# Optimization experiments

Hardware: AMD Instinct MI355X
Metric: run time of the kernel (lower is better)

## Reference

```python
import jax, jax.numpy as jnp
import numpy as np

KAPPA = 1.0
SIGMA = 0.3
EPS = 1e-5  # torch BatchNorm1d default eps


def _bn(y, g, b):
    # training-mode batch norm: biased batch statistics over the batch axis
    mu = jnp.mean(y, axis=0)
    var = jnp.mean((y - mu) ** 2, axis=0)
    return g * (y - mu) * jax.lax.rsqrt(var + EPS) + b


def _hid(x, W, b, g, be):
    # Linear -> BatchNorm1d -> ReLU
    return jax.nn.relu(_bn(x @ W + b, g, be))


def setup_inputs() -> dict:
    key = jax.random.key(0)
    ks = jax.random.split(key, 12)
    B, D, H, T = 2048, 256, 266, 51  # H = dim + 10
    S = T - 1
    sc = jnp.float32(0.1)
    f32 = jnp.float32
    inp = {}
    inp["x"] = jax.random.normal(ks[0], (B, D), f32)
    inp["dW"] = jax.random.normal(ks[1], (S, B, D), f32)   # hoisted per-step noise xi
    inp["law"] = jax.random.normal(ks[2], (S, D), f32)
    inp["timegrid"] = jnp.linspace(0.0, 1.0, T).astype(f32)
    # per-timestep MLP stacks (i_h1 / h1_h2 / h2_o)
    inp["W1"] = sc * jax.random.normal(ks[3], (S, D, H), f32)
    inp["b1"] = jnp.zeros((S, H), f32)
    inp["g1"] = jnp.ones((S, H), f32)
    inp["be1"] = jnp.zeros((S, H), f32)
    inp["W2"] = sc * jax.random.normal(ks[4], (S, H, H), f32)
    inp["b2"] = jnp.zeros((S, H), f32)
    inp["g2"] = jnp.ones((S, H), f32)
    inp["be2"] = jnp.zeros((S, H), f32)
    inp["W3"] = sc * jax.random.normal(ks[5], (S, H, D), f32)
    inp["b3"] = jnp.zeros((S, D), f32)
    # v0 network (v0_i_h1 / v0_h1_h2 / v0_h2_o, all Linear+BN+ReLU)
    inp["Wv1"] = sc * jax.random.normal(ks[6], (D, H), f32)
    inp["bv1"] = jnp.zeros((H,), f32)
    inp["gv1"] = jnp.ones((H,), f32)
    inp["bev1"] = jnp.zeros((H,), f32)
    inp["Wv2"] = sc * jax.random.normal(ks[7], (H, H), f32)
    inp["bv2"] = jnp.zeros((H,), f32)
    inp["gv2"] = jnp.ones((H,), f32)
    inp["bev2"] = jnp.zeros((H,), f32)
    inp["Wv3"] = sc * jax.random.normal(ks[8], (H, 1), f32)
    inp["bv3"] = jnp.zeros((1,), f32)
    inp["gv3"] = jnp.ones((1,), f32)
    inp["bev3"] = jnp.zeros((1,), f32)
    return inp


def reference(x, dW, law, timegrid,
              W1, b1, g1, be1, W2, b2, g2, be2, W3, b3,
              Wv1, bv1, gv1, bev1, Wv2, bv2, gv2, bev2, Wv3, bv3, gv3, bev3):
    hgrid = jnp.diff(timegrid)  # [S]
    # v0 network evaluated on the initial state (note: last stage is also Linear+BN+ReLU)
    v0 = _hid(_hid(_hid(x, Wv1, bv1, gv1, bev1), Wv2, bv2, gv2, bev2), Wv3, bv3, gv3, bev3)  # [B,1]

    def step(carry, xs):
        xc, v = carry
        w1, bb1, gg1, bbe1, w2, bb2, gg2, bbe2, w3, bb3, li, dw, h = xs
        h1 = _hid(xc, w1, bb1, gg1, bbe1)
        h2 = _hid(h1, w2, bb2, gg2, bbe2)
        grad = h2 @ w3 + bb3                                   # [B,D]
        # f = kappa^2/2 * ||x - law_i||^2 + 1/2 * ||alpha||^2,  alpha = -grad
        f = 0.5 * KAPPA ** 2 * jnp.sum((xc - li) ** 2, axis=1) + 0.5 * jnp.sum(grad ** 2, axis=1)
        noise = SIGMA * jnp.sqrt(h) * dw                       # [B,D]
        # diag(grad @ noise^T) == rowwise dot product: O(B*D) instead of O(B^2*D)
        v = v - (f * h)[:, None] + jnp.sum(grad * noise, axis=1, keepdims=True)
        xc = xc - grad * h + noise
        return (xc, v), None

    (x_final, v), _ = jax.lax.scan(
        step, (x, v0),
        (W1, b1, g1, be1, W2, b2, g2, be2, W3, b3, law, dW, hgrid))
    return v  # [B,1]; (x_final and the path are byproducts of the same scan)
```

## Files before the change

kernel.cpp:

```cpp
#include <hip/hip_runtime.h>
#include <hip/hip_bf16.h>


#define BATCH 2048
#define DD    256
#define HH    266
#define HP    272
#define SS    50
#define BN_EPS 1e-5f
#define SIG   0.3f
#define AS_STRIDE 296

#define XC_OFF 0
#define Y1_OFF 524288
#define Y2_OFF 1081344
#define V_OFF  1638400
#define S1_OFF 1640448
#define S2_OFF 1649152
#define S1V_OFF 1657856
#define S2V_OFF 1662208
#define SV_OFF  1666560
#define WQ_OFF  1666576

#define W1S 69632
#define W2S 78336
#define W3S 73728
#define W1Q_OFF 0
#define W2Q_OFF 3481600
#define W3Q_OFF 7398400
#define WV1Q_OFF 11084800
#define WV2Q_OFF 11154432

#define BAR_OFF 7283200

typedef unsigned short ushort_t;
using short8 = __attribute__((ext_vector_type(8))) short;
using f32x4  = __attribute__((ext_vector_type(4))) float;

__device__ __forceinline__ ushort_t f2b(float f) {
    unsigned u = __float_as_uint(f);
    unsigned r = u + 0x7FFF + ((u >> 16) & 1);
    return (ushort_t)(r >> 16);
}

__device__ __forceinline__ float ld_coh(const float* p) {
    return __hip_atomic_load((const float*)p, __ATOMIC_RELAXED, __HIP_MEMORY_SCOPE_AGENT);
}

__device__ __forceinline__ void prefetch16(const void* p, int n16, int tid) {
    const f32x4* q = (const f32x4*)p;
    for (int i = tid; i < n16; i += 512) {
        f32x4 t = q[i];
        asm volatile("" :: "v"(t));
    }
}

__global__ __launch_bounds__(256) void k_conv(const float* __restrict__ src,
                                              ushort_t* __restrict__ dst,
                                              int K, int N, int KT, int NT,
                                              long total) {
    long t = (long)blockIdx.x * 256 + threadIdx.x;
    if (t >= total) return;
    int per = KT * NT * 512;
    int step = (int)(t / per);
    int e = (int)(t - (long)step * per);
    int kt = e / (NT * 512);
    int r = e - kt * NT * 512;
    int nt = r / 512;
    int r2 = r & 511;
    int lane = r2 >> 3;
    int j = r2 & 7;
    int k = kt * 32 + (lane >> 4) * 8 + j;
    int n = nt * 16 + (lane & 15);
    float v = (k < K && n < N) ? src[(size_t)step * K * N + (size_t)k * N + n] : 0.f;
    dst[t] = f2b(v);
}

__global__ __launch_bounds__(256) void k_pre(float* __restrict__ ws) {
    unsigned* bar = (unsigned*)(ws + BAR_OFF);
    for (int i = threadIdx.x; i < 512; i += 256) atomicExch(bar + i, 0u);
}

__device__ __forceinline__ void grid_bar(unsigned* bar, unsigned gen, int bid) {
    __syncthreads();
    if (threadIdx.x == 0) {
        unsigned* leaf = bar + (bid & 7) * 32;
        unsigned* root = bar + 256;
        unsigned* rel  = bar + 288;
        bool done = false;
        unsigned a = __hip_atomic_fetch_add(leaf, 1u, __ATOMIC_RELAXED, __HIP_MEMORY_SCOPE_AGENT);
        if (a == gen * 32u + 31u) {
            unsigned r = __hip_atomic_fetch_add(root, 1u, __ATOMIC_RELAXED, __HIP_MEMORY_SCOPE_AGENT);
            if (r == gen * 8u + 7u) {
                __hip_atomic_store(rel, gen + 1u, __ATOMIC_RELAXED, __HIP_MEMORY_SCOPE_AGENT);
                done = true;
            }
        }
        if (!done) {
            while (__hip_atomic_load(rel, __ATOMIC_RELAXED, __HIP_MEMORY_SCOPE_AGENT) < gen + 1u)
                __builtin_amdgcn_s_sleep(1);
        }
        asm volatile("" ::: "memory");
    }
    __syncthreads();
}

__device__ __forceinline__ void compute_ac_coh(const float* __restrict__ si,
                                               const float* __restrict__ g,
                                               const float* __restrict__ be,
                                               float (*AC)[HP]) {
    int t = threadIdx.x;
    if (t < HP) {
        float a = 0.f, c = 0.f;
        if (t < HH) {
            float s = 0.f, q = 0.f;
            #pragma unroll
            for (int r = 0; r < 8; ++r) {
                s += ld_coh(si + r * 544 + t);
                q += ld_coh(si + r * 544 + 272 + t);
            }
            float mu  = s * (1.0f / 2048.0f);
            float var = q * (1.0f / 2048.0f) - mu * mu;
            float rs  = rsqrtf(fmaxf(var, 0.0f) + BN_EPS);
            a = g[t] * rs;
            c = be[t] - mu * a;
        }
        AC[0][t] = a;
        AC[1][t] = c;
    }
}

__device__ __forceinline__ void dev_lin8(
    int bid, int mode, int KT, const float* __restrict__ xsrc, int xld,
    const float* __restrict__ stats_in, const float* __restrict__ g,
    const float* __restrict__ be,
    const ushort_t* __restrict__ Wq, const float* __restrict__ bias,
    float* __restrict__ yout, float* __restrict__ stats_out,
    float* __restrict__ zero_ptr,
    ushort_t* __restrict__ As, float (*AC)[HP])
{
    const int tid  = threadIdx.x;
    const int lane = tid & 63;
    const int wv   = tid >> 6;
    const int quad = lane >> 4;
    const int l15  = lane & 15;
    const int row0 = bid * 8;

    if (zero_ptr != nullptr) {
        int z = bid * 512 + tid;
        if (z < 4352) atomicExch(zero_ptr + z, 0.0f);
    }

    if (mode == 2) { compute_ac_coh(stats_in, g, be, AC); __syncthreads(); }

    const int PAIRS = KT * 16;
    for (int idx = tid; idx < 8 * PAIRS; idx += 512) {
        int m  = idx / PAIRS;
        int kk = (idx - m * PAIRS) * 2;
        float v0, v1;
        if (mode == 2) {
            v0 = (kk < HH)   ? fmaxf(fmaf(AC[0][kk],   xsrc[(size_t)(row0+m)*xld + kk],   AC[1][kk]),   0.f) : 0.f;
            v1 = (kk+1 < HH) ? fmaxf(fmaf(AC[0][kk+1], xsrc[(size_t)(row0+m)*xld + kk+1], AC[1][kk+1]), 0.f) : 0.f;
        } else {
            v0 = xsrc[(size_t)(row0+m)*xld + kk];
            v1 = xsrc[(size_t)(row0+m)*xld + kk + 1];
        }
        ((unsigned int*)As)[m * (AS_STRIDE/2) + (kk >> 1)] =
            (unsigned int)f2b(v0) | ((unsigned int)f2b(v1) << 16);
    }
    __syncthreads();

    f32x4 acc[3];
    #pragma unroll
    for (int i = 0; i < 3; ++i) acc[i] = (f32x4){0.f, 0.f, 0.f, 0.f};

    for (int kt = 0; kt < KT; ++kt) {
        short8 af = *(const short8*)(&As[l15 * AS_STRIDE + kt * 32 + quad * 8]);
        const ushort_t* wp = Wq + ((size_t)(kt * 17 + wv)) * 512 + lane * 8;
        #pragma unroll
        for (int i = 0; i < 3; ++i) {
            if (i < 2 || wv == 0) {
                short8 bf = *(const short8*)(wp + (size_t)i * 8 * 512);
                acc[i] = __builtin_amdgcn_mfma_f32_16x16x32_bf16(af, bf, acc[i], 0, 0, 0);
            }
        }
    }

    #pragma unroll
    for (int i = 0; i < 3; ++i) {
        if (i == 2 && wv != 0) continue;
        int t = wv + 8 * i;
        int col = t * 16 + l15;
        float bj = (col < HH) ? bias[col] : 0.f;
        float y0 = acc[i][0] + bj, y1 = acc[i][1] + bj;
        float y2 = acc[i][2] + bj, y3 = acc[i][3] + bj;
        if (quad < 2) {
            yout[(size_t)(row0 + quad*4 + 0) * HP + col] = y0;
            yout[(size_t)(row0 + quad*4 + 1) * HP + col] = y1;
            yout[(size_t)(row0 + quad*4 + 2) * HP + col] = y2;
            yout[(size_t)(row0 + quad*4 + 3) * HP + col] = y3;
        }
        float sp = (quad < 2) ? (y0 + y1 + y2 + y3) : 0.f;
        float sq = (quad < 2) ? (y0*y0 + y1*y1 + y2*y2 + y3*y3) : 0.f;
        sp += __shfl_xor(sp, 16); sp += __shfl_xor(sp, 32);
        sq += __shfl_xor(sq, 16); sq += __shfl_xor(sq, 32);
        if (quad == 0 && col < HH) {
            float* spp = stats_out + (bid & 7) * 544;
            atomicAdd(spp + col, sp);
            atomicAdd(spp + 272 + col, sq);
        }
    }
}

__device__ __forceinline__ void dev_fused8(
    int bid,
    const float* __restrict__ y2g, const float* __restrict__ stats_in,
    const float* __restrict__ g2, const float* __restrict__ be2,
    const ushort_t* __restrict__ W3q, const float* __restrict__ b3,
    const float* __restrict__ law, const float* __restrict__ dWs,
    const float* __restrict__ tg, int s, int doP1,
    float* __restrict__ xc, float* __restrict__ vv, float* __restrict__ outv,
    const ushort_t* __restrict__ W1q, const float* __restrict__ b1n,
    float* __restrict__ Y1, float* __restrict__ stats_out,
    float* __restrict__ zero_ptr,
    ushort_t* __restrict__ As, float (*AC)[HP], float* __restrict__ red)
{
    const int tid  = threadIdx.x;
    const int lane = tid & 63;
    const int wv   = tid >> 6;
    const int quad = lane >> 4;
    const int l15  = lane & 15;
    const int row0 = bid * 8;

    if (zero_ptr != nullptr) {
        int z = bid * 512 + tid;
        if (z < 4352) atomicExch(zero_ptr + z, 0.0f);
    }

    compute_ac_coh(stats_in, g2, be2, AC);
    __syncthreads();

    for (int idx = tid; idx < 8 * 144; idx += 512) {
        int m  = idx / 144;
        int kk = (idx - m * 144) * 2;
        float v0 = (kk < HH)   ? fmaxf(fmaf(AC[0][kk],   y2g[(size_t)(row0+m)*HP + kk],   AC[1][kk]),   0.f) : 0.f;
        float v1 = (kk+1 < HH) ? fmaxf(fmaf(AC[0][kk+1], y2g[(size_t)(row0+m)*HP + kk+1], AC[1][kk+1]), 0.f) : 0.f;
        ((unsigned int*)As)[m * (AS_STRIDE/2) + (kk >> 1)] =
            (unsigned int)f2b(v0) | ((unsigned int)f2b(v1) << 16);
    }
    __syncthreads();

    f32x4 acc[2];
    acc[0] = (f32x4){0.f,0.f,0.f,0.f};
    acc[1] = (f32x4){0.f,0.f,0.f,0.f};
    for (int kt = 0; kt < 9; ++kt) {
        short8 af = *(const short8*)(&As[l15 * AS_STRIDE + kt * 32 + quad * 8]);
        const ushort_t* wp = W3q + ((size_t)(kt * 16 + wv)) * 512 + lane * 8;
        acc[0] = __builtin_amdgcn_mfma_f32_16x16x32_bf16(af, *(const short8*)(wp),           acc[0], 0, 0, 0);
        acc[1] = __builtin_amdgcn_mfma_f32_16x16x32_bf16(af, *(const short8*)(wp + 8 * 512), acc[1], 0, 0, 0);
    }

    const float h   = tg[s + 1] - tg[s];
    const float srt = SIG * sqrtf(h);
    float grad[2][4], xcv[2][4], dwv[2][4];
    float sxr[4] = {0,0,0,0}, sgr[4] = {0,0,0,0}, sgnr[4] = {0,0,0,0};
    #pragma unroll
    for (int i = 0; i < 2; ++i) {
        int col = (wv + 8*i) * 16 + l15;
        #pragma unroll
        for (int r = 0; r < 4; ++r) {
            float gd = acc[i][r] + b3[col];
            grad[i][r] = gd;
            xcv[i][r] = 0.f; dwv[i][r] = 0.f;
            if (quad < 2) {
                int row = row0 + quad * 4 + r;
                float xv = xc[(size_t)row * DD + col];
                float dw = dWs[(size_t)row * DD + col];
                float d  = xv - law[col];
                xcv[i][r] = xv; dwv[i][r] = dw;
                sxr[r]  = fmaf(d, d, sxr[r]);
                sgr[r]  = fmaf(gd, gd, sgr[r]);
                sgnr[r] = fmaf(gd, dw, sgnr[r]);
            }
        }
    }
    #pragma unroll
    for (int off = 1; off < 16; off <<= 1) {
        #pragma unroll
        for (int r = 0; r < 4; ++r) {
            sxr[r]  += __shfl_xor(sxr[r],  off);
            sgr[r]  += __shfl_xor(sgr[r],  off);
            sgnr[r] += __shfl_xor(sgnr[r], off);
        }
    }
    if (l15 == 0 && quad < 2) {
        #pragma unroll
        for (int r = 0; r < 4; ++r) {
            int rr = quad * 4 + r;
            red[(wv * 8 + rr) * 3 + 0] = sxr[r];
            red[(wv * 8 + rr) * 3 + 1] = sgr[r];
            red[(wv * 8 + rr) * 3 + 2] = sgnr[r];
        }
    }
    __syncthreads();

    if (tid < 8) {
        float sx = 0.f, sg = 0.f, sgn = 0.f;
        #pragma unroll
        for (int w = 0; w < 8; ++w) {
            sx  += red[(w * 8 + tid) * 3 + 0];
            sg  += red[(w * 8 + tid) * 3 + 1];
            sgn += red[(w * 8 + tid) * 3 + 2];
        }
        int row = row0 + tid;
        float f  = 0.5f * (sx + sg);
        float vn = vv[row] - f * h + srt * sgn;
        vv[row] = vn;
        if (s == SS - 1) outv[row] = vn;
    }

    #pragma unroll
    for (int i = 0; i < 2; ++i) {
        int col = (wv + 8*i) * 16 + l15;
        if (quad < 2) {
            #pragma unroll
            for (int r = 0; r < 4; ++r) {
                int row = row0 + quad * 4 + r;
                float xn = xcv[i][r] - grad[i][r] * h + srt * dwv[i][r];
                xc[(size_t)row * DD + col] = xn;
                if (doP1) As[(quad * 4 + r) * AS_STRIDE + col] = f2b(xn);
            }
        }
    }
    if (!doP1) return;
    __syncthreads();

    f32x4 acc2[3];
    #pragma unroll
    for (int i = 0; i < 3; ++i) acc2[i] = (f32x4){0.f, 0.f, 0.f, 0.f};
    for (int kt = 0; kt < 8; ++kt) {
        short8 af = *(const short8*)(&As[l15 * AS_STRIDE + kt * 32 + quad * 8]);
        const ushort_t* wp = W1q + ((size_t)(kt * 17 + wv)) * 512 + lane * 8;
        #pragma unroll
        for (int i = 0; i < 3; ++i) {
            if (i < 2 || wv == 0) {
                short8 bf = *(const short8*)(wp + (size_t)i * 8 * 512);
                acc2[i] = __builtin_amdgcn_mfma_f32_16x16x32_bf16(af, bf, acc2[i], 0, 0, 0);
            }
        }
    }
    #pragma unroll
    for (int i = 0; i < 3; ++i) {
        if (i == 2 && wv != 0) continue;
        int t = wv + 8 * i;
        int col = t * 16 + l15;
        float bj = (col < HH) ? b1n[col] : 0.f;
        float y0 = acc2[i][0] + bj, y1 = acc2[i][1] + bj;
        float y2 = acc2[i][2] + bj, y3 = acc2[i][3] + bj;
        if (quad < 2) {
            Y1[(size_t)(row0 + quad*4 + 0) * HP + col] = y0;
            Y1[(size_t)(row0 + quad*4 + 1) * HP + col] = y1;
            Y1[(size_t)(row0 + quad*4 + 2) * HP + col] = y2;
            Y1[(size_t)(row0 + quad*4 + 3) * HP + col] = y3;
        }
        float sp = (quad < 2) ? (y0 + y1 + y2 + y3) : 0.f;
        float sq = (quad < 2) ? (y0*y0 + y1*y1 + y2*y2 + y3*y3) : 0.f;
        sp += __shfl_xor(sp, 16); sp += __shfl_xor(sp, 32);
        sq += __shfl_xor(sq, 16); sq += __shfl_xor(sq, 32);
        if (quad == 0 && col < HH) {
            float* spp = stats_out + (bid & 7) * 544;
            atomicAdd(spp + col, sp);
            atomicAdd(spp + 272 + col, sq);
        }
    }
}

__device__ __forceinline__ void dev_v0l3_8(
    int bid, const float* __restrict__ y2, const float* __restrict__ stats_in,
    const float* __restrict__ gv, const float* __restrict__ bev,
    const float* __restrict__ wv3, const float* __restrict__ bv3,
    float* __restrict__ vout, float* __restrict__ sv,
    float (*AC)[HP], float* __restrict__ xtra)
{
    const int tid = threadIdx.x;
    compute_ac_coh(stats_in, gv, bev, AC);
    __syncthreads();

    const int r   = tid >> 6;
    const int ln  = tid & 63;
    const int row = bid * 8 + r;
    int k0 = ln * 5, k1 = k0 + 5;
    if (k1 > HH) k1 = HH;
    float acc = 0.0f;
    for (int k = k0; k < k1; ++k) {
        float y  = y2[(size_t)row * HP + k];
        float a2 = fmaxf(fmaf(AC[0][k], y, AC[1][k]), 0.0f);
        acc = fmaf(a2, wv3[k], acc);
    }
    #pragma unroll
    for (int off = 1; off < 64; off <<= 1) acc += __shfl_xor(acc, off);
    if (ln == 0) {
        float y = acc + bv3[0];
        vout[row] = y;
        xtra[r] = y;
        xtra[8 + r] = y * y;
    }
    __syncthreads();
    if (tid == 0) {
        float s = 0.f, q = 0.f;
        #pragma unroll
        for (int i = 0; i < 8; ++i) { s += xtra[i]; q += xtra[8 + i]; }
        atomicAdd(sv, s);
        atomicAdd(sv + 1, q);
    }
}

__device__ __forceinline__ void dev_v0fin8(int bid, float* __restrict__ v,
                                           const float* __restrict__ sv,
                                           const float* __restrict__ gv3,
                                           const float* __restrict__ bev3) {
    if (threadIdx.x < 8) {
        float s0 = ld_coh(sv);
        float s1 = ld_coh(sv + 1);
        float mu  = s0 * (1.0f / 2048.0f);
        float var = s1 * (1.0f / 2048.0f) - mu * mu;
        float rs  = rsqrtf(fmaxf(var, 0.0f) + BN_EPS);
        int row = bid * 8 + threadIdx.x;
        float y = v[row];
        v[row] = fmaxf(gv3[0] * (y - mu) * rs + bev3[0], 0.0f);
    }
}

__global__ __launch_bounds__(512) void k_persist(
    const float* __restrict__ x, const float* __restrict__ dW,
    const float* __restrict__ law, const float* __restrict__ tg,
    const float* __restrict__ b1, const float* __restrict__ g1, const float* __restrict__ be1,
    const float* __restrict__ b2, const float* __restrict__ g2, const float* __restrict__ be2,
    const float* __restrict__ b3,
    const float* __restrict__ bv1, const float* __restrict__ gv1, const float* __restrict__ bev1,
    const float* __restrict__ bv2, const float* __restrict__ gv2, const float* __restrict__ bev2,
    const float* __restrict__ Wv3, const float* __restrict__ bv3,
    const float* __restrict__ gv3, const float* __restrict__ bev3,
    float* __restrict__ ws, float* __restrict__ out)
{
    __shared__ ushort_t As[16 * AS_STRIDE];
    __shared__ float AC[2][HP];
    __shared__ float XTRA[256];

    const int bid = blockIdx.x;
    const int tid = threadIdx.x;

    float* xc  = ws + XC_OFF;
    float* Y1  = ws + Y1_OFF;
    float* Y2  = ws + Y2_OFF;
    float* V   = ws + V_OFF;
    float* S1  = ws + S1_OFF;
    float* S2  = ws + S2_OFF;
    float* S1v = ws + S1V_OFF;
    float* S2v = ws + S2V_OFF;
    float* SV  = ws + SV_OFF;
    ushort_t* WQ = (ushort_t*)(ws + WQ_OFF);
    ushort_t* W1q  = WQ + W1Q_OFF;
    ushort_t* W2q  = WQ + W2Q_OFF;
    ushort_t* W3q  = WQ + W3Q_OFF;
    ushort_t* Wv1q = WQ + WV1Q_OFF;
    ushort_t* Wv2q = WQ + WV2Q_OFF;
    unsigned* bar  = (unsigned*)(ws + BAR_OFF);

    unsigned gen = 0;
    const int sl = (bid >> 3) & 31;

    for (int i = tid; i < 2048; i += 512)
        xc[bid * 2048 + i] = x[bid * 2048 + i];
    {
        int z = bid * 512 + tid;
        if (z < 26128) atomicExch(S1 + z, 0.0f);
    }
    for (int i = tid; i < 8 * AS_STRIDE; i += 512)
        As[8 * AS_STRIDE + i] = 0;
    grid_bar(bar, gen, bid); gen++;

    dev_lin8(bid, 0, 8, x, DD, nullptr, nullptr, nullptr,
             Wv1q, bv1, Y1, S1v, nullptr, As, AC);
    grid_bar(bar, gen, bid); gen++;

    dev_lin8(bid, 2, 9, Y1, HP, S1v, gv1, bev1,
             Wv2q, bv2, Y2, S2v, nullptr, As, AC);
    grid_bar(bar, gen, bid); gen++;

    dev_v0l3_8(bid, Y2, S2v, gv2, bev2, Wv3, bv3, V, SV, AC, XTRA);
    grid_bar(bar, gen, bid); gen++;

    dev_v0fin8(bid, V, SV, gv3, bev3);
    dev_lin8(bid, 0, 8, x, DD, nullptr, nullptr, nullptr,
             W1q, b1, Y1, S1, nullptr, As, AC);
    prefetch16((const char*)W2q + sl * 4896, 306, tid);
    grid_bar(bar, gen, bid); gen++;

    for (int s = 0; s < SS; ++s) {
        int p = s & 1;
        dev_lin8(bid, 2, 9, Y1, HP, S1 + p * 4352,
                 g1 + s * HH, be1 + s * HH,
                 W2q + (size_t)s * W2S, b2 + s * HH,
                 Y2, S2 + p * 4352, S1 + (1 - p) * 4352, As, AC);
        prefetch16(dW + (size_t)s * BATCH * DD + (size_t)bid * 2048, 512, tid);
        prefetch16((const char*)(W3q + (size_t)s * W3S) + sl * 4608, 288, tid);
        if (s + 1 < SS)
            prefetch16((const char*)(W1q + (size_t)(s + 1) * W1S) + sl * 4352, 272, tid);
        grid_bar(bar, gen, bid); gen++;

        int sn = (s + 1 < SS) ? s + 1 : 0;
        dev_fused8(bid, Y2, S2 + p * 4352,
                   g2 + s * HH, be2 + s * HH,
                   W3q + (size_t)s * W3S, b3 + s * DD,
                   law + s * DD, dW + (size_t)s * BATCH * DD,
                   tg, s, (s < SS - 1) ? 1 : 0,
                   xc, V, out,
                   W1q + (size_t)sn * W1S, b1 + sn * HH,
                   Y1, S1 + ((s + 1) & 1) * 4352,
                   S2 + (1 - p) * 4352, As, AC, XTRA);
        if (s + 1 < SS)
            prefetch16((const char*)(W2q + (size_t)(s + 1) * W2S) + sl * 4896, 306, tid);
        grid_bar(bar, gen, bid); gen++;
    }
}

extern "C" void kernel_launch(void* const* d_in, const int* in_sizes, int n_in,
                              void* d_out, int out_size, void* d_ws, size_t ws_size,
                              hipStream_t stream)
{
    (void)in_sizes; (void)n_in; (void)out_size; (void)ws_size;
    const float* x    = (const float*)d_in[0];
    const float* dW   = (const float*)d_in[1];
    const float* law  = (const float*)d_in[2];
    const float* tg   = (const float*)d_in[3];
    const float* W1   = (const float*)d_in[4];
    const float* b1   = (const float*)d_in[5];
    const float* g1   = (const float*)d_in[6];
    const float* be1  = (const float*)d_in[7];
    const float* W2   = (const float*)d_in[8];
    const float* b2   = (const float*)d_in[9];
    const float* g2   = (const float*)d_in[10];
    const float* be2  = (const float*)d_in[11];
    const float* W3   = (const float*)d_in[12];
    const float* b3   = (const float*)d_in[13];
    const float* Wv1  = (const float*)d_in[14];
    const float* bv1  = (const float*)d_in[15];
    const float* gv1  = (const float*)d_in[16];
    const float* bev1 = (const float*)d_in[17];
    const float* Wv2  = (const float*)d_in[18];
    const float* bv2  = (const float*)d_in[19];
    const float* gv2  = (const float*)d_in[20];
    const float* bev2 = (const float*)d_in[21];
    const float* Wv3  = (const float*)d_in[22];
    const float* bv3  = (const float*)d_in[23];
    const float* gv3  = (const float*)d_in[24];
    const float* bev3 = (const float*)d_in[25];

    float* ws = (float*)d_ws;
    ushort_t* WQ = (ushort_t*)(ws + WQ_OFF);
    ushort_t* W1q  = WQ + W1Q_OFF;
    ushort_t* W2q  = WQ + W2Q_OFF;
    ushort_t* W3q  = WQ + W3Q_OFF;
    ushort_t* Wv1q = WQ + WV1Q_OFF;
    ushort_t* Wv2q = WQ + WV2Q_OFF;
    float* out = (float*)d_out;

    k_pre<<<1, 256, 0, stream>>>(ws);
    k_conv<<<13600, 256, 0, stream>>>(W1,  W1q,  DD, HH, 8, 17, (long)SS * W1S);
    k_conv<<<15300, 256, 0, stream>>>(W2,  W2q,  HH, HH, 9, 17, (long)SS * W2S);
    k_conv<<<14400, 256, 0, stream>>>(W3,  W3q,  HH, DD, 9, 16, (long)SS * W3S);
    k_conv<<<272,   256, 0, stream>>>(Wv1, Wv1q, DD, HH, 8, 17, (long)W1S);
    k_conv<<<306,   256, 0, stream>>>(Wv2, Wv2q, HH, HH, 9, 17, (long)W2S);

    k_persist<<<256, 512, 0, stream>>>(
        x, dW, law, tg,
        b1, g1, be1, b2, g2, be2, b3,
        bv1, gv1, bev1, bv2, gv2, bev2,
        Wv3, bv3, gv3, bev3,
        ws, out);
}
```

Measured before the change: 1.394 ms.

## Use 16-row tiles on 128 blocks and keep activations and state in LDS

Halves the persistent grid from 256 to 128 blocks, so each block now owns 16 batch rows and fills the full 16-row MFMA tile instead of wasting half of it. The per-block activations Y1/Y2 and the state xc now stay in shared memory instead of going through global workspace round trips between stages. The grid barrier leaf count changes to match 16 blocks per leaf. In exchange, LDS use per block grows, each block carries twice the row work, and only half as many CUs take part, so the per-stage latency between barriers may rise.

```diff
diff --git a/kernel.cpp b/kernel.cpp
--- a/kernel.cpp
+++ b/kernel.cpp
@@ -89,7 +89,7 @@
         unsigned* rel  = bar + 288;
         bool done = false;
         unsigned a = __hip_atomic_fetch_add(leaf, 1u, __ATOMIC_RELAXED, __HIP_MEMORY_SCOPE_AGENT);
-        if (a == gen * 32u + 31u) {
+        if (a == gen * 16u + 15u) {
             unsigned r = __hip_atomic_fetch_add(root, 1u, __ATOMIC_RELAXED, __HIP_MEMORY_SCOPE_AGENT);
             if (r == gen * 8u + 7u) {
                 __hip_atomic_store(rel, gen + 1u, __ATOMIC_RELAXED, __HIP_MEMORY_SCOPE_AGENT);
@@ -130,12 +130,15 @@
     }
 }
 
-__device__ __forceinline__ void dev_lin8(
-    int bid, int mode, int KT, const float* __restrict__ xsrc, int xld,
+__device__ __forceinline__ void dev_lin16(
+    int bid, int mode, int KT,
+    const float* __restrict__ gsrc,
+    const float* __restrict__ lsrc,
     const float* __restrict__ stats_in, const float* __restrict__ g,
     const float* __restrict__ be,
     const ushort_t* __restrict__ Wq, const float* __restrict__ bias,
-    float* __restrict__ yout, float* __restrict__ stats_out,
+    float* __restrict__ ylds,
+    float* __restrict__ stats_out,
     float* __restrict__ zero_ptr,
     ushort_t* __restrict__ As, float (*AC)[HP])
 {
@@ -144,7 +147,7 @@
     const int wv   = tid >> 6;
     const int quad = lane >> 4;
     const int l15  = lane & 15;
-    const int row0 = bid * 8;
+    const int row0 = bid * 16;
 
     if (zero_ptr != nullptr) {
         int z = bid * 512 + tid;
@@ -154,16 +157,16 @@
     if (mode == 2) { compute_ac_coh(stats_in, g, be, AC); __syncthreads(); }
 
     const int PAIRS = KT * 16;
-    for (int idx = tid; idx < 8 * PAIRS; idx += 512) {
+    for (int idx = tid; idx < 16 * PAIRS; idx += 512) {
         int m  = idx / PAIRS;
         int kk = (idx - m * PAIRS) * 2;
         float v0, v1;
         if (mode == 2) {
-            v0 = (kk < HH)   ? fmaxf(fmaf(AC[0][kk],   xsrc[(size_t)(row0+m)*xld + kk],   AC[1][kk]),   0.f) : 0.f;
-            v1 = (kk+1 < HH) ? fmaxf(fmaf(AC[0][kk+1], xsrc[(size_t)(row0+m)*xld + kk+1], AC[1][kk+1]), 0.f) : 0.f;
+            v0 = (kk < HH)   ? fmaxf(fmaf(AC[0][kk],   lsrc[m * HP + kk],   AC[1][kk]),   0.f) : 0.f;
+            v1 = (kk+1 < HH) ? fmaxf(fmaf(AC[0][kk+1], lsrc[m * HP + kk+1], AC[1][kk+1]), 0.f) : 0.f;
         } else {
-            v0 = xsrc[(size_t)(row0+m)*xld + kk];
-            v1 = xsrc[(size_t)(row0+m)*xld + kk + 1];
+            v0 = gsrc[(size_t)(row0 + m) * DD + kk];
+            v1 = gsrc[(size_t)(row0 + m) * DD + kk + 1];
         }
         ((unsigned int*)As)[m * (AS_STRIDE/2) + (kk >> 1)] =
             (unsigned int)f2b(v0) | ((unsigned int)f2b(v1) << 16);
@@ -194,14 +197,12 @@
         float bj = (col < HH) ? bias[col] : 0.f;
         float y0 = acc[i][0] + bj, y1 = acc[i][1] + bj;
         float y2 = acc[i][2] + bj, y3 = acc[i][3] + bj;
-        if (quad < 2) {
-            yout[(size_t)(row0 + quad*4 + 0) * HP + col] = y0;
-            yout[(size_t)(row0 + quad*4 + 1) * HP + col] = y1;
-            yout[(size_t)(row0 + quad*4 + 2) * HP + col] = y2;
-            yout[(size_t)(row0 + quad*4 + 3) * HP + col] = y3;
-        }
-        float sp = (quad < 2) ? (y0 + y1 + y2 + y3) : 0.f;
-        float sq = (quad < 2) ? (y0*y0 + y1*y1 + y2*y2 + y3*y3) : 0.f;
+        ylds[(quad*4 + 0) * HP + col] = y0;
+        ylds[(quad*4 + 1) * HP + col] = y1;
+        ylds[(quad*4 + 2) * HP + col] = y2;
+        ylds[(quad*4 + 3) * HP + col] = y3;
+        float sp = y0 + y1 + y2 + y3;
+        float sq = y0*y0 + y1*y1 + y2*y2 + y3*y3;
         sp += __shfl_xor(sp, 16); sp += __shfl_xor(sp, 32);
         sq += __shfl_xor(sq, 16); sq += __shfl_xor(sq, 32);
         if (quad == 0 && col < HH) {
@@ -212,16 +213,19 @@
     }
 }
 
-__device__ __forceinline__ void dev_fused8(
+__device__ __forceinline__ void dev_fused16(
     int bid,
-    const float* __restrict__ y2g, const float* __restrict__ stats_in,
+    const float* __restrict__ y2l,
+    const float* __restrict__ stats_in,
     const float* __restrict__ g2, const float* __restrict__ be2,
     const ushort_t* __restrict__ W3q, const float* __restrict__ b3,
     const float* __restrict__ law, const float* __restrict__ dWs,
     const float* __restrict__ tg, int s, int doP1,
-    float* __restrict__ xc, float* __restrict__ vv, float* __restrict__ outv,
+    float* __restrict__ xcl,
+    float* __restrict__ vv, float* __restrict__ outv,
     const ushort_t* __restrict__ W1q, const float* __restrict__ b1n,
-    float* __restrict__ Y1, float* __restrict__ stats_out,
+    float* __restrict__ y1l,
+    float* __restrict__ stats_out,
     float* __restrict__ zero_ptr,
     ushort_t* __restrict__ As, float (*AC)[HP], float* __restrict__ red)
 {
@@ -230,7 +234,7 @@
     const int wv   = tid >> 6;
     const int quad = lane >> 4;
     const int l15  = lane & 15;
-    const int row0 = bid * 8;
+    const int row0 = bid * 16;
 
     if (zero_ptr != nullptr) {
         int z = bid * 512 + tid;
@@ -240,11 +244,11 @@
     compute_ac_coh(stats_in, g2, be2, AC);
     __syncthreads();
 
-    for (int idx = tid; idx < 8 * 144; idx += 512) {
+    for (int idx = tid; idx < 16 * 144; idx += 512) {
         int m  = idx / 144;
         int kk = (idx - m * 144) * 2;
-        float v0 = (kk < HH)   ? fmaxf(fmaf(AC[0][kk],   y2g[(size_t)(row0+m)*HP + kk],   AC[1][kk]),   0.f) : 0.f;
-        float v1 = (kk+1 < HH) ? fmaxf(fmaf(AC[0][kk+1], y2g[(size_t)(row0+m)*HP + kk+1], AC[1][kk+1]), 0.f) : 0.f;
+        float v0 = (kk < HH)   ? fmaxf(fmaf(AC[0][kk],   y2l[m * HP + kk],   AC[1][kk]),   0.f) : 0.f;
+        float v1 = (kk+1 < HH) ? fmaxf(fmaf(AC[0][kk+1], y2l[m * HP + kk+1], AC[1][kk+1]), 0.f) : 0.f;
         ((unsigned int*)As)[m * (AS_STRIDE/2) + (kk >> 1)] =
             (unsigned int)f2b(v0) | ((unsigned int)f2b(v1) << 16);
     }
@@ -269,19 +273,15 @@
         int col = (wv + 8*i) * 16 + l15;
         #pragma unroll
         for (int r = 0; r < 4; ++r) {
+            int rl = quad * 4 + r;
             float gd = acc[i][r] + b3[col];
-            grad[i][r] = gd;
-            xcv[i][r] = 0.f; dwv[i][r] = 0.f;
-            if (quad < 2) {
-                int row = row0 + quad * 4 + r;
-                float xv = xc[(size_t)row * DD + col];
-                float dw = dWs[(size_t)row * DD + col];
-                float d  = xv - law[col];
-                xcv[i][r] = xv; dwv[i][r] = dw;
-                sxr[r]  = fmaf(d, d, sxr[r]);
-                sgr[r]  = fmaf(gd, gd, sgr[r]);
-                sgnr[r] = fmaf(gd, dw, sgnr[r]);
-            }
+            float xv = xcl[rl * DD + col];
+            float dw = dWs[(size_t)(row0 + rl) * DD + col];
+            float d  = xv - law[col];
+            grad[i][r] = gd; xcv[i][r] = xv; dwv[i][r] = dw;
+            sxr[r]  = fmaf(d, d, sxr[r]);
+            sgr[r]  = fmaf(gd, gd, sgr[r]);
+            sgnr[r] = fmaf(gd, dw, sgnr[r]);
         }
     }
     #pragma unroll
@@ -293,24 +293,24 @@
             sgnr[r] += __shfl_xor(sgnr[r], off);
         }
     }
-    if (l15 == 0 && quad < 2) {
+    if (l15 == 0) {
         #pragma unroll
         for (int r = 0; r < 4; ++r) {
             int rr = quad * 4 + r;
-            red[(wv * 8 + rr) * 3 + 0] = sxr[r];
-            red[(wv * 8 + rr) * 3 + 1] = sgr[r];
-            red[(wv * 8 + rr) * 3 + 2] = sgnr[r];
-        }
-    }
-    __syncthreads();
-
-    if (tid < 8) {
+            red[(wv * 16 + rr) * 3 + 0] = sxr[r];
+            red[(wv * 16 + rr) * 3 + 1] = sgr[r];
+            red[(wv * 16 + rr) * 3 + 2] = sgnr[r];
+        }
+    }
+    __syncthreads();
+
+    if (tid < 16) {
         float sx = 0.f, sg = 0.f, sgn = 0.f;
         #pragma unroll
         for (int w = 0; w < 8; ++w) {
-            sx  += red[(w * 8 + tid) * 3 + 0];
-            sg  += red[(w * 8 + tid) * 3 + 1];
-            sgn += red[(w * 8 + tid) * 3 + 2];
+            sx  += red[(w * 16 + tid) * 3 + 0];
+            sg  += red[(w * 16 + tid) * 3 + 1];
+            sgn += red[(w * 16 + tid) * 3 + 2];
         }
         int row = row0 + tid;
         float f  = 0.5f * (sx + sg);
@@ -322,14 +322,12 @@
     #pragma unroll
     for (int i = 0; i < 2; ++i) {
         int col = (wv + 8*i) * 16 + l15;
-        if (quad < 2) {
-            #pragma unroll
-            for (int r = 0; r < 4; ++r) {
-                int row = row0 + quad * 4 + r;
-                float xn = xcv[i][r] - grad[i][r] * h + srt * dwv[i][r];
-                xc[(size_t)row * DD + col] = xn;
-                if (doP1) As[(quad * 4 + r) * AS_STRIDE + col] = f2b(xn);
-            }
+        #pragma unroll
+        for (int r = 0; r < 4; ++r) {
+            int rl = quad * 4 + r;
+            float xn = xcv[i][r] - grad[i][r] * h + srt * dwv[i][r];
+            xcl[rl * DD + col] = xn;
+            if (doP1) As[rl * AS_STRIDE + col] = f2b(xn);
         }
     }
     if (!doP1) return;
@@ -357,14 +355,12 @@
         float bj = (col < HH) ? b1n[col] : 0.f;
         float y0 = acc2[i][0] + bj, y1 = acc2[i][1] + bj;
         float y2 = acc2[i][2] + bj, y3 = acc2[i][3] + bj;
-        if (quad < 2) {
-            Y1[(size_t)(row0 + quad*4 + 0) * HP + col] = y0;
-            Y1[(size_t)(row0 + quad*4 + 1) * HP + col] = y1;
-            Y1[(size_t)(row0 + quad*4 + 2) * HP + col] = y2;
-            Y1[(size_t)(row0 + quad*4 + 3) * HP + col] = y3;
-        }
-        float sp = (quad < 2) ? (y0 + y1 + y2 + y3) : 0.f;
-        float sq = (quad < 2) ? (y0*y0 + y1*y1 + y2*y2 + y3*y3) : 0.f;
+        y1l[(quad*4 + 0) * HP + col] = y0;
+        y1l[(quad*4 + 1) * HP + col] = y1;
+        y1l[(quad*4 + 2) * HP + col] = y2;
+        y1l[(quad*4 + 3) * HP + col] = y3;
+        float sp = y0 + y1 + y2 + y3;
+        float sq = y0*y0 + y1*y1 + y2*y2 + y3*y3;
         sp += __shfl_xor(sp, 16); sp += __shfl_xor(sp, 32);
         sq += __shfl_xor(sq, 16); sq += __shfl_xor(sq, 32);
         if (quad == 0 && col < HH) {
@@ -375,8 +371,8 @@
     }
 }
 
-__device__ __forceinline__ void dev_v0l3_8(
-    int bid, const float* __restrict__ y2, const float* __restrict__ stats_in,
+__device__ __forceinline__ void dev_v0l3_16(
+    int bid, const float* __restrict__ y2l, const float* __restrict__ stats_in,
     const float* __restrict__ gv, const float* __restrict__ bev,
     const float* __restrict__ wv3, const float* __restrict__ bv3,
     float* __restrict__ vout, float* __restrict__ sv,
@@ -386,46 +382,45 @@
     compute_ac_coh(stats_in, gv, bev, AC);
     __syncthreads();
 
-    const int r   = tid >> 6;
-    const int ln  = tid & 63;
-    const int row = bid * 8 + r;
-    int k0 = ln * 5, k1 = k0 + 5;
+    const int r   = tid >> 5;
+    const int ks  = tid & 31;
+    int k0 = ks * 9, k1 = k0 + 9;
     if (k1 > HH) k1 = HH;
     float acc = 0.0f;
     for (int k = k0; k < k1; ++k) {
-        float y  = y2[(size_t)row * HP + k];
+        float y  = y2l[r * HP + k];
         float a2 = fmaxf(fmaf(AC[0][k], y, AC[1][k]), 0.0f);
         acc = fmaf(a2, wv3[k], acc);
     }
     #pragma unroll
-    for (int off = 1; off < 64; off <<= 1) acc += __shfl_xor(acc, off);
-    if (ln == 0) {
+    for (int off = 1; off < 32; off <<= 1) acc += __shfl_xor(acc, off);
+    if (ks == 0) {
         float y = acc + bv3[0];
-        vout[row] = y;
+        vout[bid * 16 + r] = y;
         xtra[r] = y;
-        xtra[8 + r] = y * y;
+        xtra[16 + r] = y * y;
     }
     __syncthreads();
     if (tid == 0) {
         float s = 0.f, q = 0.f;
         #pragma unroll
-        for (int i = 0; i < 8; ++i) { s += xtra[i]; q += xtra[8 + i]; }
+        for (int i = 0; i < 16; ++i) { s += xtra[i]; q += xtra[16 + i]; }
         atomicAdd(sv, s);
         atomicAdd(sv + 1, q);
     }
 }
 
-__device__ __forceinline__ void dev_v0fin8(int bid, float* __restrict__ v,
-                                           const float* __restrict__ sv,
-                                           const float* __restrict__ gv3,
-                                           const float* __restrict__ bev3) {
-    if (threadIdx.x < 8) {
+__device__ __forceinline__ void dev_v0fin16(int bid, float* __restrict__ v,
+                                            const float* __restrict__ sv,
+                                            const float* __restrict__ gv3,
+                                            const float* __restrict__ bev3) {
+    if (threadIdx.x < 16) {
         float s0 = ld_coh(sv);
         float s1 = ld_coh(sv + 1);
         float mu  = s0 * (1.0f / 2048.0f);
         float var = s1 * (1.0f / 2048.0f) - mu * mu;
         float rs  = rsqrtf(fmaxf(var, 0.0f) + BN_EPS);
-        int row = bid * 8 + threadIdx.x;
+        int row = bid * 16 + threadIdx.x;
         float y = v[row];
         v[row] = fmaxf(gv3[0] * (y - mu) * rs + bev3[0], 0.0f);
     }
@@ -445,14 +440,14 @@
 {
     __shared__ ushort_t As[16 * AS_STRIDE];
     __shared__ float AC[2][HP];
-    __shared__ float XTRA[256];
+    __shared__ float Y1s[16 * HP];
+    __shared__ float Y2s[16 * HP];
+    __shared__ float XCs[16 * DD];
+    __shared__ float XTRA[384];
 
     const int bid = blockIdx.x;
     const int tid = threadIdx.x;
 
-    float* xc  = ws + XC_OFF;
-    float* Y1  = ws + Y1_OFF;
-    float* Y2  = ws + Y2_OFF;
     float* V   = ws + V_OFF;
     float* S1  = ws + S1_OFF;
     float* S2  = ws + S2_OFF;
@@ -468,59 +463,57 @@
     unsigned* bar  = (unsigned*)(ws + BAR_OFF);
 
     unsigned gen = 0;
-    const int sl = (bid >> 3) & 31;
-
-    for (int i = tid; i < 2048; i += 512)
-        xc[bid * 2048 + i] = x[bid * 2048 + i];
+    const int sl = (bid >> 3) & 15;
+
+    for (int i = tid; i < 16 * DD; i += 512)
+        XCs[i] = x[(size_t)bid * 16 * DD + i];
     {
         int z = bid * 512 + tid;
         if (z < 26128) atomicExch(S1 + z, 0.0f);
     }
-    for (int i = tid; i < 8 * AS_STRIDE; i += 512)
-        As[8 * AS_STRIDE + i] = 0;
     grid_bar(bar, gen, bid); gen++;
 
-    dev_lin8(bid, 0, 8, x, DD, nullptr, nullptr, nullptr,
-             Wv1q, bv1, Y1, S1v, nullptr, As, AC);
+    dev_lin16(bid, 0, 8, x, nullptr, nullptr, nullptr, nullptr,
+              Wv1q, bv1, Y1s, S1v, nullptr, As, AC);
     grid_bar(bar, gen, bid); gen++;
 
-    dev_lin8(bid, 2, 9, Y1, HP, S1v, gv1, bev1,
-             Wv2q, bv2, Y2, S2v, nullptr, As, AC);
+    dev_lin16(bid, 2, 9, nullptr, Y1s, S1v, gv1, bev1,
+              Wv2q, bv2, Y2s, S2v, nullptr, As, AC);
     grid_bar(bar, gen, bid); gen++;
 
-    dev_v0l3_8(bid, Y2, S2v, gv2, bev2, Wv3, bv3, V, SV, AC, XTRA);
+    dev_v0l3_16(bid, Y2s, S2v, gv2, bev2, Wv3, bv3, V, SV, AC, XTRA);
     grid_bar(bar, gen, bid); gen++;
 
-    dev_v0fin8(bid, V, SV, gv3, bev3);
-    dev_lin8(bid, 0, 8, x, DD, nullptr, nullptr, nullptr,
-             W1q, b1, Y1, S1, nullptr, As, AC);
-    prefetch16((const char*)W2q + sl * 4896, 306, tid);
+    dev_v0fin16(bid, V, SV, gv3, bev3);
+    dev_lin16(bid, 0, 8, x, nullptr, nullptr, nullptr, nullptr,
+              W1q, b1, Y1s, S1, nullptr, As, AC);
+    prefetch16((const char*)W2q + sl * 9792, 612, tid);
     grid_bar(bar, gen, bid); gen++;
 
     for (int s = 0; s < SS; ++s) {
         int p = s & 1;
-        dev_lin8(bid, 2, 9, Y1, HP, S1 + p * 4352,
-                 g1 + s * HH, be1 + s * HH,
-                 W2q + (size_t)s * W2S, b2 + s * HH,
-                 Y2, S2 + p * 4352, S1 + (1 - p) * 4352, As, AC);
-        prefetch16(dW + (size_t)s * BATCH * DD + (size_t)bid * 2048, 512, tid);
-        prefetch16((const char*)(W3q + (size_t)s * W3S) + sl * 4608, 288, tid);
+        dev_lin16(bid, 2, 9, nullptr, Y1s, S1 + p * 4352,
+                  g1 + s * HH, be1 + s * HH,
+                  W2q + (size_t)s * W2S, b2 + s * HH,
+                  Y2s, S2 + p * 4352, S1 + (1 - p) * 4352, As, AC);
+        prefetch16(dW + (size_t)s * BATCH * DD + (size_t)bid * 16 * DD, 1024, tid);
+        prefetch16((const char*)(W3q + (size_t)s * W3S) + sl * 9216, 576, tid);
         if (s + 1 < SS)
-            prefetch16((const char*)(W1q + (size_t)(s + 1) * W1S) + sl * 4352, 272, tid);
+            prefetch16((const char*)(W1q + (size_t)(s + 1) * W1S) + sl * 8704, 544, tid);
         grid_bar(bar, gen, bid); gen++;
 
         int sn = (s + 1 < SS) ? s + 1 : 0;
-        dev_fused8(bid, Y2, S2 + p * 4352,
-                   g2 + s * HH, be2 + s * HH,
-                   W3q + (size_t)s * W3S, b3 + s * DD,
-                   law + s * DD, dW + (size_t)s * BATCH * DD,
-                   tg, s, (s < SS - 1) ? 1 : 0,
-                   xc, V, out,
-                   W1q + (size_t)sn * W1S, b1 + sn * HH,
-                   Y1, S1 + ((s + 1) & 1) * 4352,
-                   S2 + (1 - p) * 4352, As, AC, XTRA);
+        dev_fused16(bid, Y2s, S2 + p * 4352,
+                    g2 + s * HH, be2 + s * HH,
+                    W3q + (size_t)s * W3S, b3 + s * DD,
+                    law + s * DD, dW + (size_t)s * BATCH * DD,
+                    tg, s, (s < SS - 1) ? 1 : 0,
+                    XCs, V, out,
+                    W1q + (size_t)sn * W1S, b1 + sn * HH,
+                    Y1s, S1 + ((s + 1) & 1) * 4352,
+                    S2 + (1 - p) * 4352, As, AC, XTRA);
         if (s + 1 < SS)
-            prefetch16((const char*)(W2q + (size_t)(s + 1) * W2S) + sl * 4896, 306, tid);
+            prefetch16((const char*)(W2q + (size_t)(s + 1) * W2S) + sl * 9792, 612, tid);
         grid_bar(bar, gen, bid); gen++;
     }
 }
@@ -573,7 +566,7 @@
     k_conv<<<272,   256, 0, stream>>>(Wv1, Wv1q, DD, HH, 8, 17, (long)W1S);
     k_conv<<<306,   256, 0, stream>>>(Wv2, Wv2q, HH, HH, 9, 17, (long)W2S);
 
-    k_persist<<<256, 512, 0, stream>>>(
+    k_persist<<<128, 512, 0, stream>>>(
         x, dW, law, tg,
         b1, g1, be1, b2, g2, be2, b3,
         bv1, gv1, bev1, bv2, gv2, bev2,
```

Result: faster. 1.319 ms (-5.4%).
